# Kernel optimization log

Measured on AMD Instinct MI355X. Metric: run time of the kernel, lower is better.

## Reference

```python
import jax, jax.numpy as jnp
import numpy as np

B, T, N, F = 32, 36, 10000, 3
HORIZON = 10
NUM_REGIONS = 20
NAN_RATE = 0.05


def setup_inputs() -> dict:
    key = jax.random.key(0)
    k1, k2, k3 = jax.random.split(key, 3)
    seq = jax.random.normal(k1, (B, T, N, F), dtype=jnp.float32)
    nan_mask = jax.random.uniform(k2, (B, T, N, F)) < NAN_RATE
    seq = jnp.where(nan_mask, jnp.nan, seq)
    cluster_id = jax.random.randint(k3, (N,), 0, NUM_REGIONS, dtype=jnp.int64)
    return {"seq": seq, "cluster_id": cluster_id}


def _nanmean_all(x):
    valid = ~jnp.isnan(x)
    s = jnp.where(valid, x, 0.0).sum()
    c = valid.sum().astype(x.dtype)
    return s / c


def reference(seq, cluster_id):
    x = seq[..., 0]                               # [B, T, N] speed channel
    valid = ~jnp.isnan(x)
    xz = jnp.where(valid, x, 0.0)
    cnt = valid.sum(axis=1).astype(x.dtype)       # [B, N]
    time_mean = xz.sum(axis=1) / cnt              # [B, N]; NaN if a node is all-NaN
    pred_speed = jnp.tile(time_mean[:, None, :], (1, HORIZON, 1))  # [B, 10, N]

    # per-region nanmean over nodes: segment-mean via one-hot contraction
    onehot = (cluster_id[:, None] == jnp.arange(NUM_REGIONS)).astype(x.dtype)  # [N, R]
    pvalid = ~jnp.isnan(pred_speed)
    pz = jnp.where(pvalid, pred_speed, 0.0)
    rsum = jnp.einsum('bhn,nr->bhr', pz, onehot)                     # [B, 10, R]
    rcnt = jnp.einsum('bhn,nr->bhr', pvalid.astype(x.dtype), onehot)  # [B, 10, R]
    regional = rsum / rcnt                                            # NaN if region all-NaN

    # nan_to_global_avg: replace remaining NaNs with global nanmean of each tensor
    g1 = _nanmean_all(pred_speed)
    g2 = _nanmean_all(regional)
    out_pred = jnp.where(jnp.isnan(pred_speed), g1, pred_speed)
    out_regional = jnp.where(jnp.isnan(regional), g2, regional)
    return out_pred, out_regional
```

## Files before the change

### kernel.cpp

```cpp
#include <hip/hip_runtime.h>

#define BB 32
#define TT 36
#define NN 10000
#define FF 3
#define HH 10
#define RR 20
#define NQ (NN / 4)
#define TCH 6
#define TSTEPS 6


__global__ __launch_bounds__(256) void k_partial(
        const float* __restrict__ seq,
        float4* __restrict__ psum,
        float4* __restrict__ pcnt) {
    const int b = blockIdx.y, tch = blockIdx.z;
    const int q = blockIdx.x * blockDim.x + threadIdx.x;
    if (q >= NQ) return;
    const float4* p = (const float4*)seq
        + (size_t)(b * TT + tch * TSTEPS) * (NN * FF / 4) + 3 * q;
    const size_t tstride = NN * FF / 4;
    float s0 = 0.f, s1 = 0.f, s2 = 0.f, s3 = 0.f;
    float c0 = 0.f, c1 = 0.f, c2 = 0.f, c3 = 0.f;
    #pragma unroll
    for (int t = 0; t < TSTEPS; ++t) {
        float4 a0 = p[0];
        float4 a1 = p[1];
        float4 a2 = p[2];
        p += tstride;
        float v0 = a0.x, v1 = a0.w, v2 = a1.z, v3 = a2.y;
        if (v0 == v0) { s0 += v0; c0 += 1.f; }
        if (v1 == v1) { s1 += v1; c1 += 1.f; }
        if (v2 == v2) { s2 += v2; c2 += 1.f; }
        if (v3 == v3) { s3 += v3; c3 += 1.f; }
    }
    const size_t o = (size_t)(tch * BB + b) * NQ + q;
    psum[o] = make_float4(s0, s1, s2, s3);
    pcnt[o] = make_float4(c0, c1, c2, c3);
}

__global__ __launch_bounds__(256) void k_finish(
        const float4* __restrict__ psum,
        const float4* __restrict__ pcnt,
        const int* __restrict__ cid,
        float* __restrict__ tm,
        float* __restrict__ rsum,
        float* __restrict__ rcnt,
        float* __restrict__ gsum,
        float* __restrict__ gcnt) {
    __shared__ float ls[RR];
    __shared__ float lc[RR];
    const int b = blockIdx.y;
    const int q = blockIdx.x * blockDim.x + threadIdx.x;
    if (threadIdx.x < RR) { ls[threadIdx.x] = 0.f; lc[threadIdx.x] = 0.f; }
    __syncthreads();

    float lsum = 0.f, lcnt = 0.f;
    if (q < NQ) {
        float s0 = 0.f, s1 = 0.f, s2 = 0.f, s3 = 0.f;
        float c0 = 0.f, c1 = 0.f, c2 = 0.f, c3 = 0.f;
        #pragma unroll
        for (int tch = 0; tch < TCH; ++tch) {
            const size_t o = (size_t)(tch * BB + b) * NQ + q;
            float4 ps = psum[o];
            float4 pc = pcnt[o];
            s0 += ps.x; s1 += ps.y; s2 += ps.z; s3 += ps.w;
            c0 += pc.x; c1 += pc.y; c2 += pc.z; c3 += pc.w;
        }
        const float nanf_ = __int_as_float(0x7fc00000);
        float m0 = (c0 > 0.f) ? s0 / c0 : nanf_;
        float m1 = (c1 > 0.f) ? s1 / c1 : nanf_;
        float m2 = (c2 > 0.f) ? s2 / c2 : nanf_;
        float m3 = (c3 > 0.f) ? s3 / c3 : nanf_;
        ((float4*)tm)[(size_t)b * NQ + q] = make_float4(m0, m1, m2, m3);

        const int4 r4 = ((const int4*)cid)[q];
        if (c0 > 0.f) { atomicAdd(&ls[r4.x], m0); atomicAdd(&lc[r4.x], 1.f); lsum += m0; lcnt += 1.f; }
        if (c1 > 0.f) { atomicAdd(&ls[r4.y], m1); atomicAdd(&lc[r4.y], 1.f); lsum += m1; lcnt += 1.f; }
        if (c2 > 0.f) { atomicAdd(&ls[r4.z], m2); atomicAdd(&lc[r4.z], 1.f); lsum += m2; lcnt += 1.f; }
        if (c3 > 0.f) { atomicAdd(&ls[r4.w], m3); atomicAdd(&lc[r4.w], 1.f); lsum += m3; lcnt += 1.f; }
    }

    for (int off = 32; off > 0; off >>= 1) {
        lsum += __shfl_down(lsum, off, 64);
        lcnt += __shfl_down(lcnt, off, 64);
    }
    if ((threadIdx.x & 63) == 0) {
        atomicAdd(gsum, lsum);
        atomicAdd(gcnt, lcnt);
    }

    __syncthreads();
    if (threadIdx.x < RR) {
        atomicAdd(&rsum[b * RR + threadIdx.x], ls[threadIdx.x]);
        atomicAdd(&rcnt[b * RR + threadIdx.x], lc[threadIdx.x]);
    }
}

__global__ void k_regional(const float* __restrict__ rsum,
                           const float* __restrict__ rcnt,
                           const float* __restrict__ gsum,
                           const float* __restrict__ gcnt,
                           float* __restrict__ g1out,
                           float* __restrict__ out_reg) {
    const int tid = threadIdx.x;
    __shared__ float ssum[10];
    __shared__ float scnt[10];
    __shared__ float g2s;

    float val = 0.f;
    int valid = 0;
    if (tid < BB * RR) {
        float c = rcnt[tid];
        if (c > 0.f) { val = rsum[tid] / c; valid = 1; }
    }

    float wsv = valid ? val : 0.f;
    float wcv = (float)valid;
    for (int off = 32; off > 0; off >>= 1) {
        wsv += __shfl_down(wsv, off, 64);
        wcv += __shfl_down(wcv, off, 64);
    }
    const int wave = tid >> 6;
    if ((tid & 63) == 0) { ssum[wave] = wsv; scnt[wave] = wcv; }
    __syncthreads();

    if (tid == 0) {
        float s = 0.f, c = 0.f;
        #pragma unroll
        for (int i = 0; i < 10; ++i) { s += ssum[i]; c += scnt[i]; }
        g2s = s / c;
        g1out[0] = gsum[0] / gcnt[0];
    }
    __syncthreads();

    if (tid < BB * RR) {
        const int b = tid / RR, r = tid % RR;
        const float o = valid ? val : g2s;
        #pragma unroll
        for (int h = 0; h < HH; ++h)
            out_reg[(size_t)(b * HH + h) * RR + r] = o;
    }
}

__global__ __launch_bounds__(256) void k_pred(
        const float* __restrict__ tm,
        const float* __restrict__ g1p,
        float* __restrict__ out) {
    const int b = blockIdx.y;
    const int q = blockIdx.x * blockDim.x + threadIdx.x;
    if (q >= NQ) return;
    const float g1 = g1p[0];
    float4 v = ((const float4*)tm)[(size_t)b * NQ + q];
    if (!(v.x == v.x)) v.x = g1;
    if (!(v.y == v.y)) v.y = g1;
    if (!(v.z == v.z)) v.z = g1;
    if (!(v.w == v.w)) v.w = g1;
    float4* o = (float4*)out + (size_t)b * HH * NQ + q;
    #pragma unroll
    for (int h = 0; h < HH; ++h)
        o[(size_t)h * NQ] = v;
}

extern "C" void kernel_launch(void* const* d_in, const int* in_sizes, int n_in,
                              void* d_out, int out_size, void* d_ws, size_t ws_size,
                              hipStream_t stream) {
    const float* seq = (const float*)d_in[0];
    const int*   cid = (const int*)d_in[1];
    float* out = (float*)d_out;

    float*  ws   = (float*)d_ws;
    float4* psum = (float4*)ws;
    float4* pcnt = psum + (size_t)TCH * BB * NQ;
    float*  tm   = (float*)(pcnt + (size_t)TCH * BB * NQ);
    float*  rsum = tm + (size_t)BB * NN;
    float*  rcnt = rsum + BB * RR;
    float*  gsum = rcnt + BB * RR;
    float*  gcnt = gsum + 1;
    float*  g1   = gcnt + 1;

    hipMemsetAsync(rsum, 0, (size_t)(2 * BB * RR + 2) * sizeof(float), stream);

    dim3 blk(256);
    dim3 grdA((NQ + 255) / 256, BB, TCH);
    dim3 grdB((NQ + 255) / 256, BB);
    k_partial<<<grdA, blk, 0, stream>>>(seq, psum, pcnt);
    k_finish<<<grdB, blk, 0, stream>>>(psum, pcnt, cid, tm, rsum, rcnt, gsum, gcnt);
    k_regional<<<1, 640, 0, stream>>>(rsum, rcnt, gsum, gcnt, g1,
                                      out + (size_t)BB * HH * NN);
    k_pred<<<grdB, blk, 0, stream>>>(tm, g1, out);
}
```

Before: 249.0 us.

## Replace time-chunked partial reduction with flat speed-channel extraction pass

The first kernel no longer accumulates partial sums and counts over time chunks. It now streams the whole seq tensor in a flat, wave-contiguous order and writes only the speed channel into a compact workspace. The finish kernel then does the NaN-aware time reduction over all 36 steps from that compact buffer. The aim is a more sequential read of the large input and a smaller workspace round trip (one float4 per quad per step instead of sum and count partials). In exchange, the second kernel reads more data (36 steps instead of 6 chunks × 2 buffers) and has a longer serial loop with fewer blocks.

```diff
diff --git a/kernel.cpp b/kernel.cpp
--- a/kernel.cpp
+++ b/kernel.cpp
@@ -7,42 +7,33 @@
 #define HH 10
 #define RR 20
 #define NQ (NN / 4)
-#define TCH 6
-#define TSTEPS 6
+#define TOTQ (BB * TT * NQ)
+#define EXBLOCKS 720
+#define QPW 1000
 
 
-__global__ __launch_bounds__(256) void k_partial(
-        const float* __restrict__ seq,
-        float4* __restrict__ psum,
-        float4* __restrict__ pcnt) {
-    const int b = blockIdx.y, tch = blockIdx.z;
-    const int q = blockIdx.x * blockDim.x + threadIdx.x;
-    if (q >= NQ) return;
-    const float4* p = (const float4*)seq
-        + (size_t)(b * TT + tch * TSTEPS) * (NN * FF / 4) + 3 * q;
-    const size_t tstride = NN * FF / 4;
-    float s0 = 0.f, s1 = 0.f, s2 = 0.f, s3 = 0.f;
-    float c0 = 0.f, c1 = 0.f, c2 = 0.f, c3 = 0.f;
-    #pragma unroll
-    for (int t = 0; t < TSTEPS; ++t) {
-        float4 a0 = p[0];
-        float4 a1 = p[1];
-        float4 a2 = p[2];
-        p += tstride;
-        float v0 = a0.x, v1 = a0.w, v2 = a1.z, v3 = a2.y;
-        if (v0 == v0) { s0 += v0; c0 += 1.f; }
-        if (v1 == v1) { s1 += v1; c1 += 1.f; }
-        if (v2 == v2) { s2 += v2; c2 += 1.f; }
-        if (v3 == v3) { s3 += v3; c3 += 1.f; }
+__global__ __launch_bounds__(256) void k_extract(
+        const float4* __restrict__ seq4,
+        float4* __restrict__ xz) {
+    const int wave = (blockIdx.x * 256 + threadIdx.x) >> 6;
+    const int lane = threadIdx.x & 63;
+    const int base = wave * QPW;
+    #pragma unroll 4
+    for (int k = 0; k < (QPW + 63) / 64; ++k) {
+        const int off = k * 64 + lane;
+        if (off < QPW) {
+            const int q = base + off;
+            const float4* p = seq4 + (size_t)3 * q;
+            float4 a0 = p[0];
+            float4 a1 = p[1];
+            float4 a2 = p[2];
+            xz[q] = make_float4(a0.x, a0.w, a1.z, a2.y);
+        }
     }
-    const size_t o = (size_t)(tch * BB + b) * NQ + q;
-    psum[o] = make_float4(s0, s1, s2, s3);
-    pcnt[o] = make_float4(c0, c1, c2, c3);
 }
 
 __global__ __launch_bounds__(256) void k_finish(
-        const float4* __restrict__ psum,
-        const float4* __restrict__ pcnt,
+        const float4* __restrict__ xz,
         const int* __restrict__ cid,
         float* __restrict__ tm,
         float* __restrict__ rsum,
@@ -58,15 +49,16 @@
 
     float lsum = 0.f, lcnt = 0.f;
     if (q < NQ) {
+        const float4* p = xz + (size_t)b * TT * NQ + q;
         float s0 = 0.f, s1 = 0.f, s2 = 0.f, s3 = 0.f;
         float c0 = 0.f, c1 = 0.f, c2 = 0.f, c3 = 0.f;
-        #pragma unroll
-        for (int tch = 0; tch < TCH; ++tch) {
-            const size_t o = (size_t)(tch * BB + b) * NQ + q;
-            float4 ps = psum[o];
-            float4 pc = pcnt[o];
-            s0 += ps.x; s1 += ps.y; s2 += ps.z; s3 += ps.w;
-            c0 += pc.x; c1 += pc.y; c2 += pc.z; c3 += pc.w;
+        #pragma unroll 6
+        for (int t = 0; t < TT; ++t) {
+            float4 v = p[(size_t)t * NQ];
+            if (v.x == v.x) { s0 += v.x; c0 += 1.f; }
+            if (v.y == v.y) { s1 += v.y; c1 += 1.f; }
+            if (v.z == v.z) { s2 += v.z; c2 += 1.f; }
+            if (v.w == v.w) { s3 += v.w; c3 += 1.f; }
         }
         const float nanf_ = __int_as_float(0x7fc00000);
         float m0 = (c0 > 0.f) ? s0 / c0 : nanf_;
@@ -170,10 +162,8 @@
     const int*   cid = (const int*)d_in[1];
     float* out = (float*)d_out;
 
-    float*  ws   = (float*)d_ws;
-    float4* psum = (float4*)ws;
-    float4* pcnt = psum + (size_t)TCH * BB * NQ;
-    float*  tm   = (float*)(pcnt + (size_t)TCH * BB * NQ);
+    float4* xz   = (float4*)d_ws;
+    float*  tm   = (float*)(xz + (size_t)TOTQ);
     float*  rsum = tm + (size_t)BB * NN;
     float*  rcnt = rsum + BB * RR;
     float*  gsum = rcnt + BB * RR;
@@ -183,10 +173,9 @@
     hipMemsetAsync(rsum, 0, (size_t)(2 * BB * RR + 2) * sizeof(float), stream);
 
     dim3 blk(256);
-    dim3 grdA((NQ + 255) / 256, BB, TCH);
+    k_extract<<<EXBLOCKS, blk, 0, stream>>>((const float4*)seq, xz);
     dim3 grdB((NQ + 255) / 256, BB);
-    k_partial<<<grdA, blk, 0, stream>>>(seq, psum, pcnt);
-    k_finish<<<grdB, blk, 0, stream>>>(psum, pcnt, cid, tm, rsum, rcnt, gsum, gcnt);
+    k_finish<<<grdB, blk, 0, stream>>>(xz, cid, tm, rsum, rcnt, gsum, gcnt);
     k_regional<<<1, 640, 0, stream>>>(rsum, rcnt, gsum, gcnt, g1,
                                       out + (size_t)BB * HH * NN);
     k_pred<<<grdB, blk, 0, stream>>>(tm, g1, out);
```

New measurement: 258.6 us. 1.04x slower.

## Stage seq rows through swizzled LDS with coalesced loads and register prefetch

Applied to the files above, without the earlier changes.

The first-pass reduction now loads each time row cooperatively as contiguous float4s into shared memory. It uses an XOR swizzle, and each thread then picks out the speed channel for its four nodes. The next row is prefetched into registers while the current one is processed. The time split drops from 6 to 3 chunks, which halves partial-sum traffic into the finish kernel. The cost is two barriers per time step, fewer blocks in flight, and extra LDS traffic, while the old strided per-thread float4 loads already covered the same bytes.

```diff
diff --git a/kernel.cpp b/kernel.cpp
--- a/kernel.cpp
+++ b/kernel.cpp
@@ -7,37 +7,73 @@
 #define HH 10
 #define RR 20
 #define NQ (NN / 4)
-#define TCH 6
-#define TSTEPS 6
-
-
-__global__ __launch_bounds__(256) void k_partial(
-        const float* __restrict__ seq,
+#define QPB 256
+#define FPB (QPB * 3)
+#define NSTRIP ((NQ + QPB - 1) / QPB)
+#define TSPLIT 3
+#define TPB (TT / TSPLIT)
+
+__device__ __forceinline__ int swz(int f) { return f ^ ((f >> 3) & 7); }
+
+
+__global__ __launch_bounds__(256) void k_reduce(
+        const float4* __restrict__ seq4,
         float4* __restrict__ psum,
         float4* __restrict__ pcnt) {
-    const int b = blockIdx.y, tch = blockIdx.z;
-    const int q = blockIdx.x * blockDim.x + threadIdx.x;
-    if (q >= NQ) return;
-    const float4* p = (const float4*)seq
-        + (size_t)(b * TT + tch * TSTEPS) * (NN * FF / 4) + 3 * q;
-    const size_t tstride = NN * FF / 4;
+    __shared__ float lds[FPB * 4];
+    const int strip = blockIdx.x;
+    const int b     = blockIdx.y;
+    const int z     = blockIdx.z;
+    const int tid   = threadIdx.x;
+    const int q0    = strip * QPB;
+    const int nq    = (NQ - q0 < QPB) ? (NQ - q0) : QPB;
+    const int nf4   = nq * 3;
+
+    const size_t rowstride = (size_t)NN * FF / 4;
+    const float4* base = seq4 + (size_t)(b * TT + z * TPB) * rowstride + 3 * q0;
+
+    const bool a0 = tid < nf4;
+    const bool a1 = tid + 256 < nf4;
+    const bool a2 = tid + 512 < nf4;
+
     float s0 = 0.f, s1 = 0.f, s2 = 0.f, s3 = 0.f;
     float c0 = 0.f, c1 = 0.f, c2 = 0.f, c3 = 0.f;
-    #pragma unroll
-    for (int t = 0; t < TSTEPS; ++t) {
-        float4 a0 = p[0];
-        float4 a1 = p[1];
-        float4 a2 = p[2];
-        p += tstride;
-        float v0 = a0.x, v1 = a0.w, v2 = a1.z, v3 = a2.y;
-        if (v0 == v0) { s0 += v0; c0 += 1.f; }
-        if (v1 == v1) { s1 += v1; c1 += 1.f; }
-        if (v2 == v2) { s2 += v2; c2 += 1.f; }
-        if (v3 == v3) { s3 += v3; c3 += 1.f; }
-    }
-    const size_t o = (size_t)(tch * BB + b) * NQ + q;
-    psum[o] = make_float4(s0, s1, s2, s3);
-    pcnt[o] = make_float4(c0, c1, c2, c3);
+
+    float4 r0, r1, r2;
+    if (a0) r0 = base[tid];
+    if (a1) r1 = base[tid + 256];
+    if (a2) r2 = base[tid + 512];
+
+    for (int t = 0; t < TPB; ++t) {
+        if (a0) ((float4*)lds)[swz(tid)]       = r0;
+        if (a1) ((float4*)lds)[swz(tid + 256)] = r1;
+        if (a2) ((float4*)lds)[swz(tid + 512)] = r2;
+        if (t + 1 < TPB) {
+            const float4* p = base + (size_t)(t + 1) * rowstride;
+            if (a0) r0 = p[tid];
+            if (a1) r1 = p[tid + 256];
+            if (a2) r2 = p[tid + 512];
+        }
+        __syncthreads();
+        if (tid < nq) {
+            const int w = 12 * tid;
+            float v0 = lds[4 * swz((w    ) >> 2) + ((w    ) & 3)];
+            float v1 = lds[4 * swz((w + 3) >> 2) + ((w + 3) & 3)];
+            float v2 = lds[4 * swz((w + 6) >> 2) + ((w + 6) & 3)];
+            float v3 = lds[4 * swz((w + 9) >> 2) + ((w + 9) & 3)];
+            if (v0 == v0) { s0 += v0; c0 += 1.f; }
+            if (v1 == v1) { s1 += v1; c1 += 1.f; }
+            if (v2 == v2) { s2 += v2; c2 += 1.f; }
+            if (v3 == v3) { s3 += v3; c3 += 1.f; }
+        }
+        __syncthreads();
+    }
+
+    if (tid < nq) {
+        const size_t o = (size_t)(z * BB + b) * NQ + q0 + tid;
+        psum[o] = make_float4(s0, s1, s2, s3);
+        pcnt[o] = make_float4(c0, c1, c2, c3);
+    }
 }
 
 __global__ __launch_bounds__(256) void k_finish(
@@ -61,8 +97,8 @@
         float s0 = 0.f, s1 = 0.f, s2 = 0.f, s3 = 0.f;
         float c0 = 0.f, c1 = 0.f, c2 = 0.f, c3 = 0.f;
         #pragma unroll
-        for (int tch = 0; tch < TCH; ++tch) {
-            const size_t o = (size_t)(tch * BB + b) * NQ + q;
+        for (int z = 0; z < TSPLIT; ++z) {
+            const size_t o = (size_t)(z * BB + b) * NQ + q;
             float4 ps = psum[o];
             float4 pc = pcnt[o];
             s0 += ps.x; s1 += ps.y; s2 += ps.z; s3 += ps.w;
@@ -170,10 +206,9 @@
     const int*   cid = (const int*)d_in[1];
     float* out = (float*)d_out;
 
-    float*  ws   = (float*)d_ws;
-    float4* psum = (float4*)ws;
-    float4* pcnt = psum + (size_t)TCH * BB * NQ;
-    float*  tm   = (float*)(pcnt + (size_t)TCH * BB * NQ);
+    float4* psum = (float4*)d_ws;
+    float4* pcnt = psum + (size_t)TSPLIT * BB * NQ;
+    float*  tm   = (float*)(pcnt + (size_t)TSPLIT * BB * NQ);
     float*  rsum = tm + (size_t)BB * NN;
     float*  rcnt = rsum + BB * RR;
     float*  gsum = rcnt + BB * RR;
@@ -183,9 +218,9 @@
     hipMemsetAsync(rsum, 0, (size_t)(2 * BB * RR + 2) * sizeof(float), stream);
 
     dim3 blk(256);
-    dim3 grdA((NQ + 255) / 256, BB, TCH);
+    dim3 grdA(NSTRIP, BB, TSPLIT);
     dim3 grdB((NQ + 255) / 256, BB);
-    k_partial<<<grdA, blk, 0, stream>>>(seq, psum, pcnt);
+    k_reduce<<<grdA, blk, 0, stream>>>((const float4*)seq, psum, pcnt);
     k_finish<<<grdB, blk, 0, stream>>>(psum, pcnt, cid, tm, rsum, rcnt, gsum, gcnt);
     k_regional<<<1, 640, 0, stream>>>(rsum, rcnt, gsum, gcnt, g1,
                                       out + (size_t)BB * HH * NN);
```

Measured after the change: 249.7 us. No clear change (+0.3%).
